# Kernel tuning notes

Measured on AMD Instinct MI355X. Metric: run time of the kernel, lower is better.

## Reference

```python
import jax, jax.numpy as jnp
import numpy as np

N_EMBD = 1024
HEAD_SIZE = 64


def setup_inputs() -> dict:
    key = jax.random.key(0)
    kx, kq, kk, kv = jax.random.split(key, 4)
    B, T = 8, 2048
    x = jax.random.normal(kx, (B, T, N_EMBD), dtype=jnp.float32)
    s = 1.0 / np.sqrt(N_EMBD)
    Wq = jax.random.normal(kq, (N_EMBD, HEAD_SIZE), dtype=jnp.float32) * s
    Wk = jax.random.normal(kk, (N_EMBD, HEAD_SIZE), dtype=jnp.float32) * s
    Wv = jax.random.normal(kv, (N_EMBD, HEAD_SIZE), dtype=jnp.float32) * s
    return {"x": x, "Wq": Wq, "Wk": Wk, "Wv": Wv}


def reference(x, Wq, Wk, Wv):
    # x: [B, T, C]; W*: [C, H]
    q = jnp.einsum('btc,ch->bth', x, Wq)
    k = jnp.einsum('btc,ch->bth', x, Wk)
    v = jnp.einsum('btc,ch->bth', x, Wv)
    H = q.shape[-1]
    score = jnp.einsum('bth,bsh->bts', q, k) / jnp.sqrt(jnp.asarray(H, q.dtype))
    T = score.shape[-1]
    causal = jnp.tril(jnp.ones((T, T), dtype=bool))  # [T, T]
    score = jnp.where(causal, score, -jnp.inf)
    attn = jax.nn.softmax(score, axis=-1)
    return jnp.einsum('bts,bsh->bth', attn, v)
```

## Files before the change

### kernel.cpp

```cpp
#include <hip/hip_runtime.h>

typedef __bf16 bf16;
typedef __attribute__((ext_vector_type(8))) __bf16 bf16x8;
typedef __attribute__((ext_vector_type(4))) __bf16 bf16x4;
typedef __attribute__((ext_vector_type(4))) float floatx4;

#define MFMA16(a, b, c) __builtin_amdgcn_mfma_f32_16x16x32_bf16((a), (b), (c), 0, 0, 0)

__global__ void prep_w(const float* __restrict__ Wq, const float* __restrict__ Wk,
                       const float* __restrict__ Wv, bf16* __restrict__ wTf) {
    int tid = blockIdx.x * 256 + threadIdx.x;
    int j = tid & 7;
    int l = (tid >> 3) & 15;
    int q = (tid >> 7) & 3;
    int kc = (tid >> 9) & 31;
    int mt = tid >> 14;
    int mat = mt >> 2;
    int h = ((mt & 3) << 4) + l;
    int c = kc * 32 + q * 8 + j;
    const float* W = (mat == 0) ? Wq : (mat == 1) ? Wk : Wv;
    wTf[tid] = (bf16)W[c * 64 + h];
}

#define XSTR 1032

__global__ __launch_bounds__(512, 4) void proj_qkv(const float* __restrict__ x,
                                                   const bf16* __restrict__ wTf,
                                                   bf16* __restrict__ q,
                                                   bf16* __restrict__ k,
                                                   bf16* __restrict__ vT) {
    __shared__ bf16 xs[32 * XSTR];

    const int tid = threadIdx.x;
    const int lane = tid & 63;
    const int w = tid >> 6;
    const int l15 = lane & 15;
    const int quad = lane >> 4;
    const int T0 = blockIdx.x * 32;

    {
        const int r = tid >> 4;
        const int cm = tid & 15;
        const float* gsrc = x + (size_t)(T0 + r) * 1024 + cm * 8;
        bf16* ldst = xs + r * XSTR + cm * 8;
        #pragma unroll
        for (int c = 0; c < 8; c++) {
            floatx4 u = *(const floatx4*)(gsrc + c * 128);
            floatx4 v = *(const floatx4*)(gsrc + c * 128 + 4);
            bf16x8 pk;
            pk[0] = (bf16)u[0]; pk[1] = (bf16)u[1]; pk[2] = (bf16)u[2]; pk[3] = (bf16)u[3];
            pk[4] = (bf16)v[0]; pk[5] = (bf16)v[1]; pk[6] = (bf16)v[2]; pk[7] = (bf16)v[3];
            *(bf16x8*)(ldst + c * 128) = pk;
        }
    }
    __syncthreads();

    const int mtg = w >> 1;
    const int tloc = (w & 1) * 16;

    floatx4 acc[3] = {};
    const bf16* aw0 = wTf + (size_t)(mtg * 3 + 0) * 16384 + lane * 8;
    const bf16* aw1 = wTf + (size_t)(mtg * 3 + 1) * 16384 + lane * 8;
    const bf16* aw2 = wTf + (size_t)(mtg * 3 + 2) * 16384 + lane * 8;
    const bf16* xr = xs + (tloc + l15) * XSTR + quad * 8;

    bf16x8 a0 = *(const bf16x8*)aw0;
    bf16x8 a1 = *(const bf16x8*)aw1;
    bf16x8 a2 = *(const bf16x8*)aw2;

    #pragma unroll 4
    for (int kc = 0; kc < 32; kc++) {
        bf16x8 n0 = *(const bf16x8*)(aw0 + kc * 512 + 512);
        bf16x8 n1 = *(const bf16x8*)(aw1 + kc * 512 + 512);
        bf16x8 n2 = *(const bf16x8*)(aw2 + kc * 512 + 512);
        bf16x8 bb = *(const bf16x8*)(xr + kc * 32);
        acc[0] = MFMA16(a0, bb, acc[0]);
        acc[1] = MFMA16(a1, bb, acc[1]);
        acc[2] = MFMA16(a2, bb, acc[2]);
        a0 = n0; a1 = n1; a2 = n2;
    }

    const int t = T0 + tloc + l15;
    #pragma unroll
    for (int i = 0; i < 3; i++) {
        int mtile = mtg * 3 + i;
        int mat = mtile >> 2;
        int hbase = ((mtile & 3) << 4) + (quad << 2);
        float sc = (mat == 0) ? 0.125f : 1.0f;
        bf16x4 pk;
        pk[0] = (bf16)(acc[i][0] * sc);
        pk[1] = (bf16)(acc[i][1] * sc);
        pk[2] = (bf16)(acc[i][2] * sc);
        pk[3] = (bf16)(acc[i][3] * sc);
        if (mat == 0) {
            *(bf16x4*)(q + (size_t)t * 64 + hbase) = pk;
        } else if (mat == 1) {
            *(bf16x4*)(k + (size_t)t * 64 + hbase) = pk;
        } else {
            int b = t >> 11, tt = t & 2047;
            #pragma unroll
            for (int r = 0; r < 4; r++)
                vT[(size_t)(b * 64 + hbase + r) * 2048 + tt] = pk[r];
        }
    }
}

#define KP 72

__global__ __launch_bounds__(512, 4) void flash(const bf16* __restrict__ q,
                                                const bf16* __restrict__ k,
                                                const bf16* __restrict__ vT,
                                                float* __restrict__ out) {
    __shared__ char smem[8 * 16 * 68 * 4];
    __shared__ float Ms[8][16], Ls[8][16];
    bf16* psall = (bf16*)smem;
    float* OsB = (float*)smem;

    const int b = blockIdx.x & 7;
    const int p = blockIdx.x >> 3;
    const int mtg = (p & 1) ? (127 - (p >> 1)) : (p >> 1);
    const int t0 = mtg * 16;

    const int tid = threadIdx.x;
    const int w = tid >> 6;
    const int lane = tid & 63;
    const int l15 = lane & 15;
    const int quad = lane >> 4;

    const int jd = mtg >> 2;
    const int ntt = jd + 1;
    const int js = (ntt * w) >> 3;
    const int je = (ntt * (w + 1)) >> 3;

    const bf16* qp = q + (size_t)(b * 2048 + t0 + l15) * 64 + quad * 8;
    bf16x8 qf0 = *(const bf16x8*)qp;
    bf16x8 qf1 = *(const bf16x8*)(qp + 32);

    floatx4 o[4] = {};
    float mi[4], li[4];
    #pragma unroll
    for (int r = 0; r < 4; r++) { mi[r] = -1e30f; li[r] = 0.f; }

    const int rowq = t0 + quad * 4;

    const bf16* kb0 = k + (size_t)(b * 2048 + l15) * 64 + quad * 8;
    const bf16* vb0 = vT + (size_t)(b * 64 + l15) * 2048 + quad * 8;
    bf16* psw = psall + w * 16 * KP;

    for (int jt = js; jt < je; jt++) {
        const bf16* kp = kb0 + (size_t)jt * 4096;
        floatx4 s[4] = {};
        #pragma unroll
        for (int nt = 0; nt < 4; nt++) {
            bf16x8 k0 = *(const bf16x8*)(kp + nt * 1024);
            bf16x8 k1 = *(const bf16x8*)(kp + nt * 1024 + 32);
            s[nt] = MFMA16(qf0, k0, s[nt]);
            s[nt] = MFMA16(qf1, k1, s[nt]);
        }

        if (jt == jd) {
            #pragma unroll
            for (int nt = 0; nt < 4; nt++) {
                int kv = jt * 64 + nt * 16 + l15;
                #pragma unroll
                for (int r = 0; r < 4; r++)
                    if (kv > rowq + r) s[nt][r] = -1e30f;
            }
        }

        float alpha[4];
        #pragma unroll
        for (int r = 0; r < 4; r++) {
            float mx = fmaxf(fmaxf(s[0][r], s[1][r]), fmaxf(s[2][r], s[3][r]));
            #pragma unroll
            for (int off = 1; off < 16; off <<= 1) mx = fmaxf(mx, __shfl_xor(mx, off, 64));
            float mnew = fmaxf(mi[r], mx);
            float a = __expf(mi[r] - mnew);
            mi[r] = mnew;
            float rs = 0.f;
            #pragma unroll
            for (int nt = 0; nt < 4; nt++) {
                float pv = __expf(s[nt][r] - mnew);
                s[nt][r] = pv;
                rs += pv;
            }
            #pragma unroll
            for (int off = 1; off < 16; off <<= 1) rs += __shfl_xor(rs, off, 64);
            li[r] = li[r] * a + rs;
            alpha[r] = a;
        }
        #pragma unroll
        for (int nt = 0; nt < 4; nt++)
            #pragma unroll
            for (int r = 0; r < 4; r++)
                o[nt][r] *= alpha[r];

        #pragma unroll
        for (int nt = 0; nt < 4; nt++)
            #pragma unroll
            for (int r = 0; r < 4; r++)
                psw[(quad * 4 + r) * KP + nt * 16 + l15] = (bf16)s[nt][r];

        const bf16* vp = vb0 + jt * 64;
        #pragma unroll
        for (int kc = 0; kc < 2; kc++) {
            bf16x8 af = *(const bf16x8*)(psw + l15 * KP + kc * 32 + quad * 8);
            #pragma unroll
            for (int nt = 0; nt < 4; nt++) {
                bf16x8 vv = *(const bf16x8*)(vp + nt * 32768 + kc * 32);
                o[nt] = MFMA16(af, vv, o[nt]);
            }
        }
    }

    __syncthreads();

    #pragma unroll
    for (int r = 0; r < 4; r++) {
        if (l15 == 0) { Ms[w][quad * 4 + r] = mi[r]; Ls[w][quad * 4 + r] = li[r]; }
        #pragma unroll
        for (int nt = 0; nt < 4; nt++)
            OsB[(w * 16 + quad * 4 + r) * 68 + nt * 16 + l15] = o[nt][r];
    }
    __syncthreads();

    {
        int row = tid >> 5;
        int c2 = (tid & 31) * 2;
        float Mg = -1e30f;
        #pragma unroll
        for (int u = 0; u < 8; u++) Mg = fmaxf(Mg, Ms[u][row]);
        float Lg = 0.f, v0 = 0.f, v1 = 0.f;
        #pragma unroll
        for (int u = 0; u < 8; u++) {
            float sw = __expf(Ms[u][row] - Mg);
            Lg += sw * Ls[u][row];
            const float* Or = OsB + (u * 16 + row) * 68 + c2;
            v0 += sw * Or[0];
            v1 += sw * Or[1];
        }
        float inv = 1.0f / Lg;
        float* op = out + (size_t)(b * 2048 + t0 + row) * 64 + c2;
        op[0] = v0 * inv;
        op[1] = v1 * inv;
    }
}

extern "C" void kernel_launch(void* const* d_in, const int* in_sizes, int n_in,
                              void* d_out, int out_size, void* d_ws, size_t ws_size,
                              hipStream_t stream) {
    const float* x  = (const float*)d_in[0];
    const float* Wq = (const float*)d_in[1];
    const float* Wk = (const float*)d_in[2];
    const float* Wv = (const float*)d_in[3];
    float* out = (float*)d_out;

    char* ws = (char*)d_ws;
    bf16* wTf = (bf16*)ws;
    bf16* q   = (bf16*)(ws + 394240);
    bf16* k   = (bf16*)(ws + 394240 + 2097152);
    bf16* vT  = (bf16*)(ws + 394240 + 2 * 2097152);

    hipLaunchKernelGGL(prep_w,   dim3(768),  dim3(256), 0, stream, Wq, Wk, Wv, wTf);
    hipLaunchKernelGGL(proj_qkv, dim3(512),  dim3(512), 0, stream, x, wTf, q, k, vT);
    hipLaunchKernelGGL(flash,    dim3(1024), dim3(512), 0, stream, q, k, vT, out);
}
```

Before: 157.9 us.

## Pair causal query tiles per block and transpose score MFMA layout

The flash kernel now gives each block two query tiles, a short one and its mirrored long one, and spreads the combined KV steps evenly across the 8 waves. This is meant to balance the causal workload across blocks and halve the grid. Scores are computed as K·Q so each lane holds one query row, which cuts the softmax shuffles to two per reduction and allows vectorized P stores to shared memory. The projection kernel moves to 256-thread blocks of 16 rows with double-depth weight prefetch, which raises register pressure and adds a second merge pass in flash.

Result: faster. 144.2 us (-8.6%).

```diff
diff --git a/kernel.cpp b/kernel.cpp
--- a/kernel.cpp
+++ b/kernel.cpp
@@ -24,66 +24,73 @@
 
 #define XSTR 1032
 
-__global__ __launch_bounds__(512, 4) void proj_qkv(const float* __restrict__ x,
+__global__ __launch_bounds__(256, 4) void proj_qkv(const float* __restrict__ x,
                                                    const bf16* __restrict__ wTf,
                                                    bf16* __restrict__ q,
                                                    bf16* __restrict__ k,
                                                    bf16* __restrict__ vT) {
-    __shared__ bf16 xs[32 * XSTR];
+    __shared__ bf16 xs[16 * XSTR];
 
     const int tid = threadIdx.x;
     const int lane = tid & 63;
     const int w = tid >> 6;
     const int l15 = lane & 15;
     const int quad = lane >> 4;
-    const int T0 = blockIdx.x * 32;
+    const int T0 = blockIdx.x * 16;
 
     {
         const int r = tid >> 4;
         const int cm = tid & 15;
-        const float* gsrc = x + (size_t)(T0 + r) * 1024 + cm * 8;
-        bf16* ldst = xs + r * XSTR + cm * 8;
+        const float* g = x + (size_t)(T0 + r) * 1024 + cm * 8;
+        floatx4 f[16];
         #pragma unroll
         for (int c = 0; c < 8; c++) {
-            floatx4 u = *(const floatx4*)(gsrc + c * 128);
-            floatx4 v = *(const floatx4*)(gsrc + c * 128 + 4);
+            f[2 * c]     = *(const floatx4*)(g + c * 128);
+            f[2 * c + 1] = *(const floatx4*)(g + c * 128 + 4);
+        }
+        bf16* ld = xs + r * XSTR + cm * 8;
+        #pragma unroll
+        for (int c = 0; c < 8; c++) {
             bf16x8 pk;
-            pk[0] = (bf16)u[0]; pk[1] = (bf16)u[1]; pk[2] = (bf16)u[2]; pk[3] = (bf16)u[3];
-            pk[4] = (bf16)v[0]; pk[5] = (bf16)v[1]; pk[6] = (bf16)v[2]; pk[7] = (bf16)v[3];
-            *(bf16x8*)(ldst + c * 128) = pk;
+            pk[0] = (bf16)f[2*c][0]; pk[1] = (bf16)f[2*c][1];
+            pk[2] = (bf16)f[2*c][2]; pk[3] = (bf16)f[2*c][3];
+            pk[4] = (bf16)f[2*c+1][0]; pk[5] = (bf16)f[2*c+1][1];
+            pk[6] = (bf16)f[2*c+1][2]; pk[7] = (bf16)f[2*c+1][3];
+            *(bf16x8*)(ld + c * 128) = pk;
         }
     }
     __syncthreads();
 
-    const int mtg = w >> 1;
-    const int tloc = (w & 1) * 16;
-
     floatx4 acc[3] = {};
-    const bf16* aw0 = wTf + (size_t)(mtg * 3 + 0) * 16384 + lane * 8;
-    const bf16* aw1 = wTf + (size_t)(mtg * 3 + 1) * 16384 + lane * 8;
-    const bf16* aw2 = wTf + (size_t)(mtg * 3 + 2) * 16384 + lane * 8;
-    const bf16* xr = xs + (tloc + l15) * XSTR + quad * 8;
-
-    bf16x8 a0 = *(const bf16x8*)aw0;
-    bf16x8 a1 = *(const bf16x8*)aw1;
-    bf16x8 a2 = *(const bf16x8*)aw2;
+    const bf16* aw0 = wTf + (size_t)(w * 3 + 0) * 16384 + lane * 8;
+    const bf16* aw1 = wTf + (size_t)(w * 3 + 1) * 16384 + lane * 8;
+    const bf16* aw2 = wTf + (size_t)(w * 3 + 2) * 16384 + lane * 8;
+    const bf16* xr = xs + l15 * XSTR + quad * 8;
+
+    bf16x8 a0c = *(const bf16x8*)(aw0);
+    bf16x8 a1c = *(const bf16x8*)(aw1);
+    bf16x8 a2c = *(const bf16x8*)(aw2);
+    bf16x8 a0n = *(const bf16x8*)(aw0 + 512);
+    bf16x8 a1n = *(const bf16x8*)(aw1 + 512);
+    bf16x8 a2n = *(const bf16x8*)(aw2 + 512);
 
     #pragma unroll 4
     for (int kc = 0; kc < 32; kc++) {
-        bf16x8 n0 = *(const bf16x8*)(aw0 + kc * 512 + 512);
-        bf16x8 n1 = *(const bf16x8*)(aw1 + kc * 512 + 512);
-        bf16x8 n2 = *(const bf16x8*)(aw2 + kc * 512 + 512);
+        bf16x8 p0 = *(const bf16x8*)(aw0 + (kc + 2) * 512);
+        bf16x8 p1 = *(const bf16x8*)(aw1 + (kc + 2) * 512);
+        bf16x8 p2 = *(const bf16x8*)(aw2 + (kc + 2) * 512);
         bf16x8 bb = *(const bf16x8*)(xr + kc * 32);
-        acc[0] = MFMA16(a0, bb, acc[0]);
-        acc[1] = MFMA16(a1, bb, acc[1]);
-        acc[2] = MFMA16(a2, bb, acc[2]);
-        a0 = n0; a1 = n1; a2 = n2;
-    }
-
-    const int t = T0 + tloc + l15;
+        acc[0] = MFMA16(a0c, bb, acc[0]);
+        acc[1] = MFMA16(a1c, bb, acc[1]);
+        acc[2] = MFMA16(a2c, bb, acc[2]);
+        a0c = a0n; a1c = a1n; a2c = a2n;
+        a0n = p0;  a1n = p1;  a2n = p2;
+    }
+
+    const int t = T0 + l15;
     #pragma unroll
     for (int i = 0; i < 3; i++) {
-        int mtile = mtg * 3 + i;
+        int mtile = w * 3 + i;
         int mat = mtile >> 2;
         int hbase = ((mtile & 3) << 4) + (quad << 2);
         float sc = (mat == 0) ? 0.125f : 1.0f;
@@ -105,21 +112,25 @@
     }
 }
 
-#define KP 72
+#define KP2 72
+#define OH 68
 
 __global__ __launch_bounds__(512, 4) void flash(const bf16* __restrict__ q,
                                                 const bf16* __restrict__ k,
                                                 const bf16* __restrict__ vT,
                                                 float* __restrict__ out) {
-    __shared__ char smem[8 * 16 * 68 * 4];
+    __shared__ char smem[8 * 16 * OH * 4];
     __shared__ float Ms[8][16], Ls[8][16];
     bf16* psall = (bf16*)smem;
-    float* OsB = (float*)smem;
+    float* Os = (float*)smem;
 
     const int b = blockIdx.x & 7;
     const int p = blockIdx.x >> 3;
-    const int mtg = (p & 1) ? (127 - (p >> 1)) : (p >> 1);
-    const int t0 = mtg * 16;
+    const int t0A = p * 16;
+    const int t0B = (127 - p) * 16;
+    const int nttA = (p >> 2) + 1;
+    const int nttB = ((127 - p) >> 2) + 1;
+    const int L = nttA + nttB;
 
     const int tid = threadIdx.x;
     const int w = tid >> 6;
@@ -127,123 +138,131 @@
     const int l15 = lane & 15;
     const int quad = lane >> 4;
 
-    const int jd = mtg >> 2;
-    const int ntt = jd + 1;
-    const int js = (ntt * w) >> 3;
-    const int je = (ntt * (w + 1)) >> 3;
-
-    const bf16* qp = q + (size_t)(b * 2048 + t0 + l15) * 64 + quad * 8;
-    bf16x8 qf0 = *(const bf16x8*)qp;
-    bf16x8 qf1 = *(const bf16x8*)(qp + 32);
-
-    floatx4 o[4] = {};
-    float mi[4], li[4];
+    const int s0 = (L * w) >> 3;
+    const int s1 = (L * (w + 1)) >> 3;
+
+    const bf16* kbase = k + (size_t)(b * 2048 + l15) * 64 + quad * 8;
+    const bf16* vbase = vT + (size_t)(b * 64 + l15) * 2048 + quad * 8;
+    bf16* psw = psall + w * 16 * KP2;
+
+    const bf16* qpA = q + (size_t)(b * 2048 + t0A + l15) * 64 + quad * 8;
+    const bf16* qpB = q + (size_t)(b * 2048 + t0B + l15) * 64 + quad * 8;
+
+    floatx4 oA[4] = {}, oB[4] = {};
+    float miA = -1e30f, liA = 0.f, miB = -1e30f, liB = 0.f;
+
+#define KV_STEP(jtv, isdiag, t0v, qf0v, qf1v, mi_, li_, o_)                          \
+    {                                                                                 \
+        const bf16* kp = kbase + (size_t)(jtv) * 4096;                                \
+        floatx4 stt[4];                                                               \
+        _Pragma("unroll") for (int mt = 0; mt < 4; mt++) {                            \
+            floatx4 z = {};                                                           \
+            bf16x8 ka0 = *(const bf16x8*)(kp + mt * 1024);                            \
+            bf16x8 ka1 = *(const bf16x8*)(kp + mt * 1024 + 32);                       \
+            z = MFMA16(ka0, qf0v, z);                                                 \
+            z = MFMA16(ka1, qf1v, z);                                                 \
+            stt[mt] = z;                                                              \
+        }                                                                             \
+        if (isdiag) {                                                                 \
+            _Pragma("unroll") for (int mt = 0; mt < 4; mt++)                          \
+                _Pragma("unroll") for (int r = 0; r < 4; r++) {                       \
+                    int kv = (jtv) * 64 + mt * 16 + quad * 4 + r;                     \
+                    if (kv > (t0v) + l15) stt[mt][r] = -1e30f;                        \
+                }                                                                     \
+        }                                                                             \
+        float mx = fmaxf(fmaxf(fmaxf(stt[0][0], stt[0][1]), fmaxf(stt[0][2], stt[0][3])),  \
+                         fmaxf(fmaxf(stt[1][0], stt[1][1]), fmaxf(stt[1][2], stt[1][3]))); \
+        mx = fmaxf(mx, fmaxf(fmaxf(fmaxf(stt[2][0], stt[2][1]), fmaxf(stt[2][2], stt[2][3])),  \
+                             fmaxf(fmaxf(stt[3][0], stt[3][1]), fmaxf(stt[3][2], stt[3][3])))); \
+        mx = fmaxf(mx, __shfl_xor(mx, 16, 64));                                       \
+        mx = fmaxf(mx, __shfl_xor(mx, 32, 64));                                       \
+        float mnew = fmaxf(mi_, mx);                                                  \
+        float aa = __expf(mi_ - mnew);                                                \
+        mi_ = mnew;                                                                   \
+        float rs = 0.f;                                                               \
+        _Pragma("unroll") for (int mt = 0; mt < 4; mt++)                              \
+            _Pragma("unroll") for (int r = 0; r < 4; r++) {                           \
+                float pv = __expf(stt[mt][r] - mnew);                                 \
+                stt[mt][r] = pv;                                                      \
+                rs += pv;                                                             \
+            }                                                                         \
+        rs += __shfl_xor(rs, 16, 64);                                                 \
+        rs += __shfl_xor(rs, 32, 64);                                                 \
+        li_ = li_ * aa + rs;                                                          \
+        _Pragma("unroll") for (int mt = 0; mt < 4; mt++)                              \
+            _Pragma("unroll") for (int r = 0; r < 4; r++) o_[mt][r] *= aa;            \
+        _Pragma("unroll") for (int mt = 0; mt < 4; mt++) {                            \
+            bf16x4 pk;                                                                \
+            pk[0] = (bf16)stt[mt][0]; pk[1] = (bf16)stt[mt][1];                       \
+            pk[2] = (bf16)stt[mt][2]; pk[3] = (bf16)stt[mt][3];                       \
+            *(bf16x4*)(psw + l15 * KP2 + mt * 16 + quad * 4) = pk;                    \
+        }                                                                             \
+        const bf16* vp = vbase + (jtv) * 64;                                          \
+        _Pragma("unroll") for (int kc = 0; kc < 2; kc++) {                            \
+            bf16x8 pb = *(const bf16x8*)(psw + l15 * KP2 + kc * 32 + quad * 8);       \
+            _Pragma("unroll") for (int mt = 0; mt < 4; mt++) {                        \
+                bf16x8 va = *(const bf16x8*)(vp + mt * 32768 + kc * 32);              \
+                o_[mt] = MFMA16(va, pb, o_[mt]);                                      \
+            }                                                                         \
+        }                                                                             \
+    }
+
+    {
+        const int eA = (s1 < nttA) ? s1 : nttA;
+        if (s0 < eA) {
+            bf16x8 qf0 = *(const bf16x8*)qpA;
+            bf16x8 qf1 = *(const bf16x8*)(qpA + 32);
+            for (int s = s0; s < eA; s++) {
+                KV_STEP(s, (s == nttA - 1), t0A, qf0, qf1, miA, liA, oA);
+            }
+        }
+    }
+    {
+        const int sB = (s0 > nttA) ? s0 : nttA;
+        if (sB < s1) {
+            bf16x8 qf0 = *(const bf16x8*)qpB;
+            bf16x8 qf1 = *(const bf16x8*)(qpB + 32);
+            for (int s = sB; s < s1; s++) {
+                KV_STEP(s - nttA, (s == L - 1), t0B, qf0, qf1, miB, liB, oB);
+            }
+        }
+    }
+
     #pragma unroll
-    for (int r = 0; r < 4; r++) { mi[r] = -1e30f; li[r] = 0.f; }
-
-    const int rowq = t0 + quad * 4;
-
-    const bf16* kb0 = k + (size_t)(b * 2048 + l15) * 64 + quad * 8;
-    const bf16* vb0 = vT + (size_t)(b * 64 + l15) * 2048 + quad * 8;
-    bf16* psw = psall + w * 16 * KP;
-
-    for (int jt = js; jt < je; jt++) {
-        const bf16* kp = kb0 + (size_t)jt * 4096;
-        floatx4 s[4] = {};
+    for (int tile = 0; tile < 2; tile++) {
+        __syncthreads();
+        float mi = tile ? miB : miA;
+        float li = tile ? liB : liA;
+        if (lane < 16) { Ms[w][lane] = mi; Ls[w][lane] = li; }
         #pragma unroll
-        for (int nt = 0; nt < 4; nt++) {
-            bf16x8 k0 = *(const bf16x8*)(kp + nt * 1024);
-            bf16x8 k1 = *(const bf16x8*)(kp + nt * 1024 + 32);
-            s[nt] = MFMA16(qf0, k0, s[nt]);
-            s[nt] = MFMA16(qf1, k1, s[nt]);
-        }
-
-        if (jt == jd) {
+        for (int mt = 0; mt < 4; mt++) {
+            floatx4 ov = tile ? oB[mt] : oA[mt];
+            *(floatx4*)(Os + (w * 16 + l15) * OH + mt * 16 + quad * 4) = ov;
+        }
+        __syncthreads();
+        {
+            int qq = tid >> 5;
+            int h2 = (tid & 31) * 2;
+            float Mg = -1e30f;
             #pragma unroll
-            for (int nt = 0; nt < 4; nt++) {
-                int kv = jt * 64 + nt * 16 + l15;
-                #pragma unroll
-                for (int r = 0; r < 4; r++)
-                    if (kv > rowq + r) s[nt][r] = -1e30f;
+            for (int u = 0; u < 8; u++) Mg = fmaxf(Mg, Ms[u][qq]);
+            float Lg = 0.f, v0 = 0.f, v1 = 0.f;
+            #pragma unroll
+            for (int u = 0; u < 8; u++) {
+                float sw = __expf(Ms[u][qq] - Mg);
+                Lg += sw * Ls[u][qq];
+                const float* Or = Os + (u * 16 + qq) * OH + h2;
+                v0 += sw * Or[0];
+                v1 += sw * Or[1];
             }
-        }
-
-        float alpha[4];
-        #pragma unroll
-        for (int r = 0; r < 4; r++) {
-            float mx = fmaxf(fmaxf(s[0][r], s[1][r]), fmaxf(s[2][r], s[3][r]));
-            #pragma unroll
-            for (int off = 1; off < 16; off <<= 1) mx = fmaxf(mx, __shfl_xor(mx, off, 64));
-            float mnew = fmaxf(mi[r], mx);
-            float a = __expf(mi[r] - mnew);
-            mi[r] = mnew;
-            float rs = 0.f;
-            #pragma unroll
-            for (int nt = 0; nt < 4; nt++) {
-                float pv = __expf(s[nt][r] - mnew);
-                s[nt][r] = pv;
-                rs += pv;
-            }
-            #pragma unroll
-            for (int off = 1; off < 16; off <<= 1) rs += __shfl_xor(rs, off, 64);
-            li[r] = li[r] * a + rs;
-            alpha[r] = a;
-        }
-        #pragma unroll
-        for (int nt = 0; nt < 4; nt++)
-            #pragma unroll
-            for (int r = 0; r < 4; r++)
-                o[nt][r] *= alpha[r];
-
-        #pragma unroll
-        for (int nt = 0; nt < 4; nt++)
-            #pragma unroll
-            for (int r = 0; r < 4; r++)
-                psw[(quad * 4 + r) * KP + nt * 16 + l15] = (bf16)s[nt][r];
-
-        const bf16* vp = vb0 + jt * 64;
-        #pragma unroll
-        for (int kc = 0; kc < 2; kc++) {
-            bf16x8 af = *(const bf16x8*)(psw + l15 * KP + kc * 32 + quad * 8);
-            #pragma unroll
-            for (int nt = 0; nt < 4; nt++) {
-                bf16x8 vv = *(const bf16x8*)(vp + nt * 32768 + kc * 32);
-                o[nt] = MFMA16(af, vv, o[nt]);
-            }
-        }
-    }
-
-    __syncthreads();
-
-    #pragma unroll
-    for (int r = 0; r < 4; r++) {
-        if (l15 == 0) { Ms[w][quad * 4 + r] = mi[r]; Ls[w][quad * 4 + r] = li[r]; }
-        #pragma unroll
-        for (int nt = 0; nt < 4; nt++)
-            OsB[(w * 16 + quad * 4 + r) * 68 + nt * 16 + l15] = o[nt][r];
-    }
-    __syncthreads();
-
-    {
-        int row = tid >> 5;
-        int c2 = (tid & 31) * 2;
-        float Mg = -1e30f;
-        #pragma unroll
-        for (int u = 0; u < 8; u++) Mg = fmaxf(Mg, Ms[u][row]);
-        float Lg = 0.f, v0 = 0.f, v1 = 0.f;
-        #pragma unroll
-        for (int u = 0; u < 8; u++) {
-            float sw = __expf(Ms[u][row] - Mg);
-            Lg += sw * Ls[u][row];
-            const float* Or = OsB + (u * 16 + row) * 68 + c2;
-            v0 += sw * Or[0];
-            v1 += sw * Or[1];
-        }
-        float inv = 1.0f / Lg;
-        float* op = out + (size_t)(b * 2048 + t0 + row) * 64 + c2;
-        op[0] = v0 * inv;
-        op[1] = v1 * inv;
-    }
+            float inv = 1.0f / Lg;
+            int t0v = tile ? t0B : t0A;
+            float* op = out + (size_t)(b * 2048 + t0v + qq) * 64 + h2;
+            op[0] = v0 * inv;
+            op[1] = v1 * inv;
+        }
+    }
+#undef KV_STEP
 }
 
 extern "C" void kernel_launch(void* const* d_in, const int* in_sizes, int n_in,
@@ -257,11 +276,11 @@
 
     char* ws = (char*)d_ws;
     bf16* wTf = (bf16*)ws;
-    bf16* q   = (bf16*)(ws + 394240);
-    bf16* k   = (bf16*)(ws + 394240 + 2097152);
-    bf16* vT  = (bf16*)(ws + 394240 + 2 * 2097152);
+    bf16* q   = (bf16*)(ws + 397312);
+    bf16* k   = (bf16*)(ws + 397312 + 2097152);
+    bf16* vT  = (bf16*)(ws + 397312 + 2 * 2097152);
 
     hipLaunchKernelGGL(prep_w,   dim3(768),  dim3(256), 0, stream, Wq, Wk, Wv, wTf);
-    hipLaunchKernelGGL(proj_qkv, dim3(512),  dim3(512), 0, stream, x, wTf, q, k, vT);
-    hipLaunchKernelGGL(flash,    dim3(1024), dim3(512), 0, stream, q, k, vT, out);
-}
+    hipLaunchKernelGGL(proj_qkv, dim3(1024), dim3(256), 0, stream, x, wTf, q, k, vT);
+    hipLaunchKernelGGL(flash,    dim3(512),  dim3(512), 0, stream, q, k, vT, out);
+}
```
